# Kernel tuning notes

Hardware: AMD Instinct MI355X
Metric: run time of the kernel (lower is better)

## Reference

```python
import jax, jax.numpy as jnp
import numpy as np

# LIF time constants (hardcoded in the torch module)
TIME_STEP = 0.001
ALPHA = float(np.exp(-TIME_STEP / 0.005))  # synapse decay
BETA = float(np.exp(-TIME_STEP / 0.01))    # membrane decay
EPS = 1e-8
SG_SCALE = 100.0  # surrogate-gradient sharpness (SurrogateHeaviside)

B, CIN, T, H, W = 8, 2, 64, 64, 64
COUT = 32
KS = (3, 3, 3)

@jax.custom_vjp
def spike_fn(x):
    return (x > 0).astype(x.dtype)

def _spike_fwd(x):
    return spike_fn(x), x

def _spike_bwd(x, g):
    sig = jax.nn.sigmoid(SG_SCALE * x)
    return (g * SG_SCALE * sig * (1.0 - sig),)

spike_fn.defvjp(_spike_fwd, _spike_bwd)

def setup_inputs() -> dict:
    key = jax.random.key(0)
    kx, kw, kb = jax.random.split(key, 3)
    x = jax.random.normal(kx, (B, CIN, T, H, W), dtype=jnp.float32)
    w_std = 0.15 * np.sqrt(1.0 / (CIN * np.prod(KS)))
    w = jax.random.normal(kw, (COUT, CIN, *KS), dtype=jnp.float32) * w_std
    b = jnp.clip(1.0 + 0.01 * jax.random.normal(kb, (COUT,), dtype=jnp.float32), 0.0, None)
    return {"x": x, "w": w, "b": b}

def reference(x, w, b):
    # conv3d, padding = ceil((k-1)*dilation/2) = 1 per dim, stride 1
    conv_x = jax.lax.conv_general_dilated(
        x, w, window_strides=(1, 1, 1),
        padding=((1, 1), (1, 1), (1, 1)),
        dimension_numbers=("NCDHW", "OIDHW", "NCDHW"))
    conv_x = conv_x[:, :, :, :H, :W]  # crop to output_shape (no-op for stride 1)

    # lateral-connection matrix and per-channel weight norm
    d = jnp.einsum("oixyz,pixyz->op", w, w)           # [Cout, Cout]
    norm = jnp.sum(w * w, axis=(1, 2, 3, 4))          # [Cout]
    inv_norm = (1.0 / (norm + EPS))[None, :, None, None]
    bias = b[None, :, None, None]

    zeros = jnp.zeros((B, COUT, H, W), dtype=x.dtype)

    def step(carry, inp_t):
        mem, syn, spk = carry
        rst = jnp.einsum("bchw,cd->bdhw", spk, d)     # lateral reset
        new_syn = ALPHA * syn + inp_t
        new_mem = BETA * mem + syn - rst              # uses OLD syn
        mthr = new_mem * inv_norm - bias
        new_spk = spike_fn(mthr)
        return (new_mem, new_syn, new_spk), new_spk

    conv_t = jnp.moveaxis(conv_x, 2, 0)               # [T, B, C, H, W]
    _, spk_rec = jax.lax.scan(step, (zeros, zeros, zeros), conv_t)
    return jnp.moveaxis(spk_rec, 0, 2)                # [B, C, T, H, W]
```

## Files before the change

kernel.cpp:

```cpp
#include <hip/hip_runtime.h>

#define ALPHA_F ((float)0.8187307530779818)
#define BETA_F  ((float)0.9048374180359595)

__global__ __launch_bounds__(512) void snn_v7(
    const float* __restrict__ x, const float* __restrict__ wq,
    const float* __restrict__ bvec, float* __restrict__ out)
{
    __shared__ float wl[32][54];
    __shared__ float wps[3][32][18];
    __shared__ __align__(16) float Dl[32][32];
    __shared__ float invl[32];
    __shared__ float biasl[32];
    __shared__ unsigned char msk[2][64][8];

    const int tid = threadIdx.x;
    const int w  = tid & 63;
    const int wv = tid >> 6;
    const int c0 = wv * 4;
    const int idx = blockIdx.x;
    const int b = idx >> 6;
    const int h = ((idx & 7) << 3) | ((idx >> 3) & 7);

    for (int i = tid; i < 1728; i += 512) wl[i / 54][i % 54] = wq[i];
    __syncthreads();
    for (int i = tid; i < 1728; i += 512) {
        int c = i / 54, j = i % 54;
        int kt = j / 18, jj = j % 18;
        int ci = jj & 1, r = jj >> 1;
        int kh = r / 3, kw = r % 3;
        wps[kt][c][jj] = wl[c][ci * 27 + kt * 9 + kh * 3 + kw];
    }
    for (int e = tid; e < 1024; e += 512) {
        int cp = e >> 5, c = e & 31;
        float s = 0.f;
        #pragma unroll
        for (int k = 0; k < 54; ++k) s = fmaf(wl[cp][k], wl[c][k], s);
        Dl[cp][c] = s;
    }
    __syncthreads();
    if (tid < 32) {
        float s = 0.f;
        #pragma unroll
        for (int k = 0; k < 54; ++k)
            s = __fadd_rn(s, __fmul_rn(wl[tid][k], wl[tid][k]));
        invl[tid] = 1.0f / __fadd_rn(s, 1e-8f);
        biasl[tid] = bvec[tid];
    }
    __syncthreads();

    float mem[4], syn[4], S1[4], S2[4];
    #pragma unroll
    for (int cl = 0; cl < 4; ++cl) { mem[cl] = 0.f; syn[cl] = 0.f; }
    unsigned mask = 0u;

    float inv_r[4], bias_r[4];
    #pragma unroll
    for (int cl = 0; cl < 4; ++cl) { inv_r[cl] = invl[c0 + cl]; bias_r[cl] = biasl[c0 + cl]; }

    const size_t xb = (size_t)b * 524288;
    const size_t ob = (size_t)b * 8388608 + (size_t)c0 * 262144 + (size_t)h * 64 + (size_t)w;

    float xv[18];
    #define GATHER(TT, POK)                                                    \
    {                                                                          \
        const int tt = (TT);                                                   \
        _Pragma("unroll")                                                      \
        for (int kh = 0; kh < 3; ++kh) {                                       \
            int hh = h + kh - 1;                                               \
            bool hok = (unsigned)hh < 64u;                                     \
            int hhc = hok ? hh : 0;                                            \
            bool ok = (POK) && hok;                                            \
            const float* rp0 = x + xb + (size_t)(tt * 4096 + hhc * 64);        \
            const float* rp1 = rp0 + 262144;                                   \
            float a0 = rp0[(w > 0) ? (w - 1) : 0];                             \
            float a1 = rp0[w];                                                 \
            float a2 = rp0[(w < 63) ? (w + 1) : 63];                           \
            float b0 = rp1[(w > 0) ? (w - 1) : 0];                             \
            float b1 = rp1[w];                                                 \
            float b2 = rp1[(w < 63) ? (w + 1) : 63];                           \
            xv[(kh * 3 + 0) * 2 + 0] = (ok && w > 0)  ? a0 : 0.f;              \
            xv[(kh * 3 + 0) * 2 + 1] = (ok && w > 0)  ? b0 : 0.f;              \
            xv[(kh * 3 + 1) * 2 + 0] = ok ? a1 : 0.f;                          \
            xv[(kh * 3 + 1) * 2 + 1] = ok ? b1 : 0.f;                          \
            xv[(kh * 3 + 2) * 2 + 0] = (ok && w < 63) ? a2 : 0.f;              \
            xv[(kh * 3 + 2) * 2 + 1] = (ok && w < 63) ? b2 : 0.f;              \
        }                                                                      \
    }

    GATHER(0, true);
    #pragma unroll
    for (int cl = 0; cl < 4; ++cl) {
        float a = 0.f;
        #pragma unroll
        for (int jj = 0; jj < 18; ++jj) a = fmaf(xv[jj], wps[1][c0 + cl][jj], a);
        S2[cl] = a;
        float s = 0.f;
        #pragma unroll
        for (int jj = 0; jj < 18; ++jj) s = fmaf(xv[jj], wps[0][c0 + cl][jj], s);
        S1[cl] = s;
    }

    for (int t = 0; t < 64; ++t) {
        float rst[4] = {0.f, 0.f, 0.f, 0.f};
        if (__ballot(mask != 0u)) {
            #pragma unroll
            for (int cp = 0; cp < 32; ++cp) {
                float s = ((mask >> cp) & 1u) ? 1.0f : 0.0f;
                const float4 dv = *(const float4*)&Dl[cp][c0];
                rst[0] = fmaf(s, dv.x, rst[0]);
                rst[1] = fmaf(s, dv.y, rst[1]);
                rst[2] = fmaf(s, dv.z, rst[2]);
                rst[3] = fmaf(s, dv.w, rst[3]);
            }
        }

        const int par = t & 1;
        unsigned nib = 0u;
        #pragma unroll
        for (int cl = 0; cl < 4; ++cl) {
            float bm = __fmul_rn(BETA_F, mem[cl]);
            float bs = __fadd_rn(bm, syn[cl]);
            mem[cl] = __fsub_rn(bs, rst[cl]);
            float mthr = __fsub_rn(__fmul_rn(mem[cl], inv_r[cl]), bias_r[cl]);
            bool s = mthr > 0.f;
            nib |= (s ? 1u : 0u) << cl;
            out[ob + (size_t)cl * 262144 + (size_t)t * 4096] = s ? 1.0f : 0.0f;
        }
        msk[par][w][wv] = (unsigned char)nib;

        GATHER((t < 63) ? (t + 1) : 63, (t < 63));

        float acc[4];
        #pragma unroll
        for (int cl = 0; cl < 4; ++cl) {
            float a = S2[cl];
            #pragma unroll
            for (int jj = 0; jj < 18; ++jj) a = fmaf(xv[jj], wps[2][c0 + cl][jj], a);
            acc[cl] = a;
        }
        #pragma unroll
        for (int cl = 0; cl < 4; ++cl) {
            float a = S1[cl];
            #pragma unroll
            for (int jj = 0; jj < 18; ++jj) a = fmaf(xv[jj], wps[1][c0 + cl][jj], a);
            S2[cl] = a;
            float s = 0.f;
            #pragma unroll
            for (int jj = 0; jj < 18; ++jj) s = fmaf(xv[jj], wps[0][c0 + cl][jj], s);
            S1[cl] = s;
        }
        #pragma unroll
        for (int cl = 0; cl < 4; ++cl)
            syn[cl] = __fadd_rn(__fmul_rn(ALPHA_F, syn[cl]), acc[cl]);

        __syncthreads();
        const uint2 mv = *(const uint2*)&msk[par][w][0];
        unsigned lo = (mv.x | (mv.x >> 4)) & 0x00FF00FFu;
        lo = (lo | (lo >> 8)) & 0xFFFFu;
        unsigned hi = (mv.y | (mv.y >> 4)) & 0x00FF00FFu;
        hi = (hi | (hi >> 8)) & 0xFFFFu;
        mask = lo | (hi << 16);
    }
    #undef GATHER
}

extern "C" void kernel_launch(void* const* d_in, const int* in_sizes, int n_in,
                              void* d_out, int out_size, void* d_ws, size_t ws_size,
                              hipStream_t stream) {
    const float* x  = (const float*)d_in[0];
    const float* wq = (const float*)d_in[1];
    const float* bv = (const float*)d_in[2];
    for (int i = 0; i < n_in; ++i) {
        int sz = in_sizes[i];
        if (sz == 8 * 2 * 64 * 64 * 64) x  = (const float*)d_in[i];
        else if (sz == 32 * 2 * 27)     wq = (const float*)d_in[i];
        else if (sz == 32)              bv = (const float*)d_in[i];
    }
    float* out = (float*)d_out;
    snn_v7<<<512, 512, 0, stream>>>(x, wq, bv, out);
}
```

Baseline: 405.8 us.

## Stage input rows in shared memory and share spikes as floats

Each thread now issues one coalesced global load per step into a double-buffered shared tile of the three input rows (with zero halo), replacing the 18 redundant global gathers per thread. The thread then reads its 3x3x2 neighbourhood from LDS. The packed bitmask spike exchange is replaced by a float spike array in shared memory that the reset loop reads directly. This removes the bit-unpacking work and the ballot skip, so the 32-term reset FMA loop now always runs and adds 32 LDS reads per step.

```diff
diff --git a/kernel.cpp b/kernel.cpp
--- a/kernel.cpp
+++ b/kernel.cpp
@@ -3,7 +3,7 @@
 #define ALPHA_F ((float)0.8187307530779818)
 #define BETA_F  ((float)0.9048374180359595)
 
-__global__ __launch_bounds__(512) void snn_v7(
+__global__ __launch_bounds__(512) void snn_v8(
     const float* __restrict__ x, const float* __restrict__ wq,
     const float* __restrict__ bvec, float* __restrict__ out)
 {
@@ -12,7 +12,8 @@
     __shared__ __align__(16) float Dl[32][32];
     __shared__ float invl[32];
     __shared__ float biasl[32];
-    __shared__ unsigned char msk[2][64][8];
+    __shared__ float spk[2][32][64];
+    __shared__ float xl[2][2][3][66];
 
     const int tid = threadIdx.x;
     const int w  = tid & 63;
@@ -38,7 +39,12 @@
         for (int k = 0; k < 54; ++k) s = fmaf(wl[cp][k], wl[c][k], s);
         Dl[cp][c] = s;
     }
-    __syncthreads();
+    for (int i = tid; i < 4096; i += 512) ((float*)spk)[i] = 0.f;
+    if (tid < 24) {
+        int p = tid / 12, r = tid % 12;
+        int ci = r / 6, kh = (r % 6) >> 1, end = r & 1;
+        xl[p][ci][kh][end ? 65 : 0] = 0.f;
+    }
     if (tid < 32) {
         float s = 0.f;
         #pragma unroll
@@ -47,66 +53,69 @@
         invl[tid] = 1.0f / __fadd_rn(s, 1e-8f);
         biasl[tid] = bvec[tid];
     }
+
+    const size_t xb = (size_t)b * 524288;
+    const int sci = (tid < 384) ? (tid / 192) : 0;
+    const int skh = (tid < 384) ? ((tid % 192) / 64) : 0;
+    const int sw  = tid & 63;
+    const int shh = h + skh - 1;
+    const bool srow_ok = (tid < 384) && ((unsigned)shh < 64u);
+    const size_t sbase = xb + (size_t)sci * 262144 + (size_t)shh * 64 + sw;
+
+    {
+        float v = srow_ok ? x[sbase] : 0.f;
+        if (tid < 384) xl[0][sci][skh][1 + sw] = v;
+    }
     __syncthreads();
-
-    float mem[4], syn[4], S1[4], S2[4];
-    #pragma unroll
-    for (int cl = 0; cl < 4; ++cl) { mem[cl] = 0.f; syn[cl] = 0.f; }
-    unsigned mask = 0u;
 
     float inv_r[4], bias_r[4];
     #pragma unroll
     for (int cl = 0; cl < 4; ++cl) { inv_r[cl] = invl[c0 + cl]; bias_r[cl] = biasl[c0 + cl]; }
 
-    const size_t xb = (size_t)b * 524288;
-    const size_t ob = (size_t)b * 8388608 + (size_t)c0 * 262144 + (size_t)h * 64 + (size_t)w;
-
     float xv[18];
-    #define GATHER(TT, POK)                                                    \
+    #define LOADXV(P)                                                          \
     {                                                                          \
-        const int tt = (TT);                                                   \
         _Pragma("unroll")                                                      \
-        for (int kh = 0; kh < 3; ++kh) {                                       \
-            int hh = h + kh - 1;                                               \
-            bool hok = (unsigned)hh < 64u;                                     \
-            int hhc = hok ? hh : 0;                                            \
-            bool ok = (POK) && hok;                                            \
-            const float* rp0 = x + xb + (size_t)(tt * 4096 + hhc * 64);        \
-            const float* rp1 = rp0 + 262144;                                   \
-            float a0 = rp0[(w > 0) ? (w - 1) : 0];                             \
-            float a1 = rp0[w];                                                 \
-            float a2 = rp0[(w < 63) ? (w + 1) : 63];                           \
-            float b0 = rp1[(w > 0) ? (w - 1) : 0];                             \
-            float b1 = rp1[w];                                                 \
-            float b2 = rp1[(w < 63) ? (w + 1) : 63];                           \
-            xv[(kh * 3 + 0) * 2 + 0] = (ok && w > 0)  ? a0 : 0.f;              \
-            xv[(kh * 3 + 0) * 2 + 1] = (ok && w > 0)  ? b0 : 0.f;              \
-            xv[(kh * 3 + 1) * 2 + 0] = ok ? a1 : 0.f;                          \
-            xv[(kh * 3 + 1) * 2 + 1] = ok ? b1 : 0.f;                          \
-            xv[(kh * 3 + 2) * 2 + 0] = (ok && w < 63) ? a2 : 0.f;              \
-            xv[(kh * 3 + 2) * 2 + 1] = (ok && w < 63) ? b2 : 0.f;              \
+        for (int ci = 0; ci < 2; ++ci) {                                       \
+            _Pragma("unroll")                                                  \
+            for (int kh = 0; kh < 3; ++kh) {                                   \
+                const float* row = &xl[P][ci][kh][w];                          \
+                xv[(kh * 3 + 0) * 2 + ci] = row[0];                            \
+                xv[(kh * 3 + 1) * 2 + ci] = row[1];                            \
+                xv[(kh * 3 + 2) * 2 + ci] = row[2];                            \
+            }                                                                  \
         }                                                                      \
     }
 
-    GATHER(0, true);
+    float S1[4], S2[4], mem[4], syn[4];
+    LOADXV(0);
     #pragma unroll
     for (int cl = 0; cl < 4; ++cl) {
-        float a = 0.f;
+        float a = 0.f, s = 0.f;
         #pragma unroll
         for (int jj = 0; jj < 18; ++jj) a = fmaf(xv[jj], wps[1][c0 + cl][jj], a);
         S2[cl] = a;
-        float s = 0.f;
         #pragma unroll
         for (int jj = 0; jj < 18; ++jj) s = fmaf(xv[jj], wps[0][c0 + cl][jj], s);
         S1[cl] = s;
+        mem[cl] = 0.f; syn[cl] = 0.f;
     }
 
+    const size_t ob = (size_t)b * 8388608 + (size_t)c0 * 262144 + (size_t)h * 64 + (size_t)w;
+
     for (int t = 0; t < 64; ++t) {
+        const int pcur = t & 1;
+        const int pnxt = (t + 1) & 1;
+
+        float sval = 0.f;
+        if (srow_ok && t < 63) sval = x[sbase + (size_t)(t + 1) * 4096];
+
         float rst[4] = {0.f, 0.f, 0.f, 0.f};
-        if (__ballot(mask != 0u)) {
+        {
+            const float* sp = &spk[pnxt][0][w];
             #pragma unroll
             for (int cp = 0; cp < 32; ++cp) {
-                float s = ((mask >> cp) & 1u) ? 1.0f : 0.0f;
+                float s = sp[cp * 64];
                 const float4 dv = *(const float4*)&Dl[cp][c0];
                 rst[0] = fmaf(s, dv.x, rst[0]);
                 rst[1] = fmaf(s, dv.y, rst[1]);
@@ -115,22 +124,22 @@
             }
         }
 
-        const int par = t & 1;
-        unsigned nib = 0u;
         #pragma unroll
         for (int cl = 0; cl < 4; ++cl) {
             float bm = __fmul_rn(BETA_F, mem[cl]);
             float bs = __fadd_rn(bm, syn[cl]);
             mem[cl] = __fsub_rn(bs, rst[cl]);
             float mthr = __fsub_rn(__fmul_rn(mem[cl], inv_r[cl]), bias_r[cl]);
-            bool s = mthr > 0.f;
-            nib |= (s ? 1u : 0u) << cl;
-            out[ob + (size_t)cl * 262144 + (size_t)t * 4096] = s ? 1.0f : 0.0f;
+            float sf = (mthr > 0.f) ? 1.0f : 0.0f;
+            spk[pcur][c0 + cl][w] = sf;
+            out[ob + (size_t)cl * 262144 + (size_t)t * 4096] = sf;
         }
-        msk[par][w][wv] = (unsigned char)nib;
 
-        GATHER((t < 63) ? (t + 1) : 63, (t < 63));
+        if (tid < 384) xl[pnxt][sci][skh][1 + sw] = sval;
 
+        __syncthreads();
+
+        LOADXV(pnxt);
         float acc[4];
         #pragma unroll
         for (int cl = 0; cl < 4; ++cl) {
@@ -141,11 +150,10 @@
         }
         #pragma unroll
         for (int cl = 0; cl < 4; ++cl) {
-            float a = S1[cl];
+            float a = S1[cl], s = 0.f;
             #pragma unroll
             for (int jj = 0; jj < 18; ++jj) a = fmaf(xv[jj], wps[1][c0 + cl][jj], a);
             S2[cl] = a;
-            float s = 0.f;
             #pragma unroll
             for (int jj = 0; jj < 18; ++jj) s = fmaf(xv[jj], wps[0][c0 + cl][jj], s);
             S1[cl] = s;
@@ -153,16 +161,8 @@
         #pragma unroll
         for (int cl = 0; cl < 4; ++cl)
             syn[cl] = __fadd_rn(__fmul_rn(ALPHA_F, syn[cl]), acc[cl]);
-
-        __syncthreads();
-        const uint2 mv = *(const uint2*)&msk[par][w][0];
-        unsigned lo = (mv.x | (mv.x >> 4)) & 0x00FF00FFu;
-        lo = (lo | (lo >> 8)) & 0xFFFFu;
-        unsigned hi = (mv.y | (mv.y >> 4)) & 0x00FF00FFu;
-        hi = (hi | (hi >> 8)) & 0xFFFFu;
-        mask = lo | (hi << 16);
     }
-    #undef GATHER
+    #undef LOADXV
 }
 
 extern "C" void kernel_launch(void* const* d_in, const int* in_sizes, int n_in,
@@ -178,5 +178,5 @@
         else if (sz == 32)              bv = (const float*)d_in[i];
     }
     float* out = (float*)d_out;
-    snn_v7<<<512, 512, 0, stream>>>(x, wq, bv, out);
+    snn_v8<<<512, 512, 0, stream>>>(x, wq, bv, out);
 }
```

Measured after the change: 336.8 us. -17.0%, faster.
